# Performance work log

Hardware: AMD Instinct MI355X
Metric: run time of the kernel (lower is better)

## Reference

```python
import jax, jax.numpy as jnp
import numpy as np

LOCAL_RANGE = 7  # module default local_range
NUM_HEADS = 8


def setup_inputs() -> dict:
    key = jax.random.key(0)
    k1, k2, k3 = jax.random.split(key, 3)
    B, S, D = 2, 2048, 512
    hidden_states = jax.random.normal(k1, (B, S, D), dtype=jnp.float32)
    scale = 1.0 / (D ** 0.5)
    Wq = jax.random.normal(k2, (D, D), dtype=jnp.float32) * scale
    Wk = jax.random.normal(k3, (D, D), dtype=jnp.float32) * scale
    return {"hidden_states": hidden_states, "Wq": Wq, "Wk": Wk}


def reference(hidden_states, Wq, Wk):
    B, S, D = hidden_states.shape
    H = NUM_HEADS
    dh = D // H
    # inner attention: only attn_weights matter (context_layer is overwritten)
    q = (hidden_states @ Wq).reshape(B, S, H, dh).transpose(0, 2, 1, 3)  # [B,H,S,dh]
    k = (hidden_states @ Wk).reshape(B, S, H, dh).transpose(0, 2, 1, 3)  # [B,H,S,dh]
    scores = jnp.einsum('bhid,bhjd->bhij', q, k) / (dh ** 0.5)          # [B,H,S,S]
    attn_weights = jax.nn.softmax(scores, axis=-1)
    # band-diagonal local mask: |i-j| <= local_range (vectorized form of the python loop)
    idx = jnp.arange(S)
    band = (jnp.abs(idx[:, None] - idx[None, :]) <= LOCAL_RANGE).astype(attn_weights.dtype)  # [S,S]
    local_w = attn_weights * band
    local_w = local_w / (jnp.sum(local_w, axis=-1, keepdims=True) + 1e-6)
    # context = matmul(local_attn_weights, hidden_states): per-head contraction
    context = jnp.einsum('bhij,bjd->bhid', local_w, hidden_states)       # [B,H,S,D]
    return context
```

## Files before the change

### kernel.cpp

```cpp
#include <hip/hip_runtime.h>
#include <hip/hip_bf16.h>
#include <math.h>

#define SEQ   2048
#define DIM   512
#define NH    8
#define DH    64
#define LR    7

typedef __bf16 bf16_t;
typedef __bf16 bf16x8 __attribute__((ext_vector_type(8)));
typedef float  f32x4  __attribute__((ext_vector_type(4)));

__global__ __launch_bounds__(256) void wt_convert(
    const float* __restrict__ Wq, const float* __restrict__ Wk,
    bf16_t* __restrict__ Wt)
{
    __shared__ float tile[64][68];
    const int tid = threadIdx.x;
    const int k0 = blockIdx.x * 64;
    const int n0 = blockIdx.y * 64;
    const float* W = (n0 < DIM) ? Wq : Wk;
    const int nn0 = n0 & (DIM - 1);

    #pragma unroll
    for (int ph = 0; ph < 4; ++ph) {
        const int kk = ph * 16 + (tid >> 4);
        const int nn = (tid & 15) * 4;
        const float4 v = *(const float4*)(W + (size_t)(k0 + kk) * DIM + nn0 + nn);
        tile[kk][nn + 0] = v.x; tile[kk][nn + 1] = v.y;
        tile[kk][nn + 2] = v.z; tile[kk][nn + 3] = v.w;
    }
    __syncthreads();
    #pragma unroll
    for (int ph = 0; ph < 4; ++ph) {
        const int nn = ph * 16 + (tid >> 4);
        const int kk = (tid & 15) * 4;
        union { bf16_t b[4]; ushort4 u; } cv;
        #pragma unroll
        for (int u = 0; u < 4; ++u) cv.b[u] = (bf16_t)tile[kk + u][nn];
        *(ushort4*)(Wt + (size_t)(n0 + nn) * DIM + k0 + kk) = cv.u;
    }
}

__global__ __launch_bounds__(256) void qk_gemm_mfma(
    const float* __restrict__ A,
    const bf16_t* __restrict__ Bt,
    float* __restrict__ C)
{
    __shared__ bf16_t As[128][32];
    __shared__ bf16_t Bs[128][32];

    const int tid  = threadIdx.x;
    const int wave = tid >> 6;
    const int lane = tid & 63;
    const int l15  = lane & 15;
    const int quad = lane >> 4;
    const int wm   = (wave >> 1) * 64;
    const int wn   = (wave & 1) * 64;
    const int m0   = blockIdx.x * 128;
    const int n0   = blockIdx.y * 128;

    const int sm = tid >> 1;
    const int kh = (tid & 1) * 16;

    f32x4 acc[4][4] = {};

    for (int k0 = 0; k0 < DIM; k0 += 32) {
        {
            const float* ap = A + (size_t)(m0 + sm) * DIM + k0 + kh;
            const float4 f0 = *(const float4*)(ap + 0);
            const float4 f1 = *(const float4*)(ap + 4);
            const float4 f2 = *(const float4*)(ap + 8);
            const float4 f3 = *(const float4*)(ap + 12);
            union { bf16_t b[8]; uint4 u; } c0, c1;
            c0.b[0]=(bf16_t)f0.x; c0.b[1]=(bf16_t)f0.y; c0.b[2]=(bf16_t)f0.z; c0.b[3]=(bf16_t)f0.w;
            c0.b[4]=(bf16_t)f1.x; c0.b[5]=(bf16_t)f1.y; c0.b[6]=(bf16_t)f1.z; c0.b[7]=(bf16_t)f1.w;
            c1.b[0]=(bf16_t)f2.x; c1.b[1]=(bf16_t)f2.y; c1.b[2]=(bf16_t)f2.z; c1.b[3]=(bf16_t)f2.w;
            c1.b[4]=(bf16_t)f3.x; c1.b[5]=(bf16_t)f3.y; c1.b[6]=(bf16_t)f3.z; c1.b[7]=(bf16_t)f3.w;
            *(uint4*)&As[sm][kh + 0] = c0.u;
            *(uint4*)&As[sm][kh + 8] = c1.u;
        }
        {
            const uint4* bp = (const uint4*)(Bt + (size_t)(n0 + sm) * DIM + k0 + kh);
            *(uint4*)&Bs[sm][kh + 0] = bp[0];
            *(uint4*)&Bs[sm][kh + 8] = bp[1];
        }
        __syncthreads();

        bf16x8 af[4], bfv[4];
        #pragma unroll
        for (int t = 0; t < 4; ++t)
            af[t] = *(const bf16x8*)&As[wm + t * 16 + l15][quad * 8];
        #pragma unroll
        for (int t = 0; t < 4; ++t)
            bfv[t] = *(const bf16x8*)&Bs[wn + t * 16 + l15][quad * 8];

        #pragma unroll
        for (int mi = 0; mi < 4; ++mi)
            #pragma unroll
            for (int ni = 0; ni < 4; ++ni)
                acc[mi][ni] = __builtin_amdgcn_mfma_f32_16x16x32_bf16(
                    af[mi], bfv[ni], acc[mi][ni], 0, 0, 0);
        __syncthreads();
    }

    #pragma unroll
    for (int mi = 0; mi < 4; ++mi) {
        #pragma unroll
        for (int ni = 0; ni < 4; ++ni) {
            const int col = n0 + wn + ni * 16 + l15;
            #pragma unroll
            for (int r = 0; r < 4; ++r) {
                const int row = m0 + wm + mi * 16 + quad * 4 + r;
                C[(size_t)row * 1024 + col] = acc[mi][ni][r];
            }
        }
    }
}

#define TI 8
#define NROW (TI + 2 * LR)

__global__ __launch_bounds__(256) void local_attn2(
    const float* __restrict__ hs,
    const float* __restrict__ qk,
    float* __restrict__ out)
{
    __shared__ float hst[NROW][DIM + 4];
    __shared__ float sw[NH * TI][17];
    __shared__ float wn[NH * TI][17];

    const int tid = threadIdx.x;
    const int i0  = blockIdx.x * TI;
    const int b   = blockIdx.y;

    {
        const float4* hs4 = (const float4*)(hs + (size_t)b * SEQ * DIM);
        #pragma unroll
        for (int it = 0; it < (NROW * DIM / 4) / 256; ++it) {
            const int idx = it * 256 + tid;
            const int r   = idx >> 7;
            const int c4  = idx & 127;
            int jg = i0 - LR + r;
            jg = jg < 0 ? 0 : (jg > SEQ - 1 ? SEQ - 1 : jg);
            const float4 v = hs4[(size_t)jg * (DIM / 4) + c4];
            *(float4*)&hst[r][c4 * 4] = v;
        }
    }

    {
        const int pair = tid >> 2;
        const int h  = pair >> 3;
        const int ii = pair & (TI - 1);
        const int jq = tid & 3;
        const int i  = i0 + ii;
        const float4* qp = (const float4*)(qk + (size_t)(b * SEQ + i) * 1024 + h * DH);
        float4 q[DH / 4];
        #pragma unroll
        for (int u = 0; u < DH / 4; ++u) q[u] = qp[u];
        #pragma unroll
        for (int j = jq * 4; j < jq * 4 + 4 && j < 15; ++j) {
            const int jg = i - LR + j;
            float s = -1e30f;
            if (jg >= 0 && jg < SEQ) {
                const float4* kp = (const float4*)(qk + (size_t)(b * SEQ + jg) * 1024 + DIM + h * DH);
                float a = 0.f;
                #pragma unroll
                for (int u = 0; u < DH / 4; ++u) {
                    const float4 kv = kp[u];
                    a += q[u].x * kv.x + q[u].y * kv.y + q[u].z * kv.z + q[u].w * kv.w;
                }
                s = a * 0.125f;
            }
            sw[pair][j] = s;
        }
    }
    __syncthreads();

    if (tid < NH * TI) {
        float v[15], m = -1e30f;
        #pragma unroll
        for (int j = 0; j < 15; ++j) { v[j] = sw[tid][j]; m = fmaxf(m, v[j]); }
        float sum = 0.f;
        #pragma unroll
        for (int j = 0; j < 15; ++j) { v[j] = __expf(v[j] - m); sum += v[j]; }
        const float inv = 1.f / sum;
        #pragma unroll
        for (int j = 0; j < 15; ++j) wn[tid][j] = v[j] * inv;
    }
    __syncthreads();

    {
        const int h  = tid >> 5;
        const int iq = (tid >> 4) & 1;
        const int dg = tid & 15;

        float wreg[4][15];
        #pragma unroll
        for (int t = 0; t < 4; ++t) {
            const int pair = h * TI + iq * 4 + t;
            #pragma unroll
            for (int j = 0; j < 15; ++j) wreg[t][j] = wn[pair][j];
        }

        const int r0 = iq * 4;
        float* op = out + ((size_t)(b * NH + h) * SEQ + i0 + iq * 4) * DIM;

        for (int c = 0; c < DIM / 64; ++c) {
            const int dbase = c * 64 + dg * 4;
            float4 a0 = {0,0,0,0}, a1 = {0,0,0,0}, a2 = {0,0,0,0}, a3 = {0,0,0,0};
            #pragma unroll
            for (int rr = 0; rr < 18; ++rr) {
                const float4 v = *(const float4*)&hst[r0 + rr][dbase];
                if (rr <= 14) {
                    const float w = wreg[0][rr];
                    a0.x += w * v.x; a0.y += w * v.y; a0.z += w * v.z; a0.w += w * v.w;
                }
                if (rr >= 1 && rr <= 15) {
                    const float w = wreg[1][rr - 1];
                    a1.x += w * v.x; a1.y += w * v.y; a1.z += w * v.z; a1.w += w * v.w;
                }
                if (rr >= 2 && rr <= 16) {
                    const float w = wreg[2][rr - 2];
                    a2.x += w * v.x; a2.y += w * v.y; a2.z += w * v.z; a2.w += w * v.w;
                }
                if (rr >= 3) {
                    const float w = wreg[3][rr - 3];
                    a3.x += w * v.x; a3.y += w * v.y; a3.z += w * v.z; a3.w += w * v.w;
                }
            }
            *(float4*)(op + (size_t)0 * DIM + dbase) = a0;
            *(float4*)(op + (size_t)1 * DIM + dbase) = a1;
            *(float4*)(op + (size_t)2 * DIM + dbase) = a2;
            *(float4*)(op + (size_t)3 * DIM + dbase) = a3;
        }
    }
}

extern "C" void kernel_launch(void* const* d_in, const int* in_sizes, int n_in,
                              void* d_out, int out_size, void* d_ws, size_t ws_size,
                              hipStream_t stream)
{
    const float* hs = (const float*)d_in[0];
    const float* Wq = (const float*)d_in[1];
    const float* Wk = (const float*)d_in[2];
    float* out = (float*)d_out;

    const int B = in_sizes[0] / (SEQ * DIM);
    const int M = B * SEQ;

    bf16_t* Wt = (bf16_t*)d_ws;
    float*  qk = (float*)((char*)d_ws + (1 << 20));

    wt_convert<<<dim3(DIM / 64, 2 * DIM / 64), 256, 0, stream>>>(Wq, Wk, Wt);
    qk_gemm_mfma<<<dim3(M / 128, 1024 / 128), 256, 0, stream>>>(hs, Wt, qk);
    local_attn2<<<dim3(SEQ / TI, B), 256, 0, stream>>>(hs, qk, out);
}
```

Before: 127.9 us.

## Pre-convert activations to bf16, use direct global-to-LDS loads, stage Q/K band in LDS

Merges weight transposition with a new pass that converts hidden_states to bf16, so the QK GEMM reads bf16 activations through global_load_lds direct-to-LDS copies instead of converting fp32 in the loop. The GEMM M-tile is halved to 64 rows, which doubles the number of blocks. The local attention kernel stages the K band and the Q rows in shared memory so the score loop reads LDS instead of global memory, then reuses the same buffer for the hidden-state band. The cost is an extra 4 MB bf16 write and read, plus more LDS use per attention block.

```diff
diff --git a/kernel.cpp b/kernel.cpp
--- a/kernel.cpp
+++ b/kernel.cpp
@@ -12,14 +12,33 @@
 typedef __bf16 bf16x8 __attribute__((ext_vector_type(8)));
 typedef float  f32x4  __attribute__((ext_vector_type(4)));
 
-__global__ __launch_bounds__(256) void wt_convert(
+typedef __attribute__((address_space(3))) void  lds_void;
+typedef __attribute__((address_space(1))) const void gbl_cvoid;
+
+__global__ __launch_bounds__(256) void prep(
+    const float* __restrict__ hs,
     const float* __restrict__ Wq, const float* __restrict__ Wk,
+    bf16_t* __restrict__ hsb,
     bf16_t* __restrict__ Wt)
 {
+    const int tid = threadIdx.x;
+    const int bx  = blockIdx.x;
+
+    if (bx < 1024) {
+        const size_t base = ((size_t)bx * 256 + tid) * 8;
+        const float4 f0 = *(const float4*)(hs + base);
+        const float4 f1 = *(const float4*)(hs + base + 4);
+        union { bf16_t b[8]; uint4 u; } cv;
+        cv.b[0]=(bf16_t)f0.x; cv.b[1]=(bf16_t)f0.y; cv.b[2]=(bf16_t)f0.z; cv.b[3]=(bf16_t)f0.w;
+        cv.b[4]=(bf16_t)f1.x; cv.b[5]=(bf16_t)f1.y; cv.b[6]=(bf16_t)f1.z; cv.b[7]=(bf16_t)f1.w;
+        *(uint4*)(hsb + base) = cv.u;
+        return;
+    }
+
     __shared__ float tile[64][68];
-    const int tid = threadIdx.x;
-    const int k0 = blockIdx.x * 64;
-    const int n0 = blockIdx.y * 64;
+    const int t  = bx - 1024;
+    const int k0 = (t & 7) * 64;
+    const int n0 = (t >> 3) * 64;
     const float* W = (n0 < DIM) ? Wq : Wk;
     const int nn0 = n0 & (DIM - 1);
 
@@ -44,11 +63,11 @@
 }
 
 __global__ __launch_bounds__(256) void qk_gemm_mfma(
-    const float* __restrict__ A,
+    const bf16_t* __restrict__ A,
     const bf16_t* __restrict__ Bt,
     float* __restrict__ C)
 {
-    __shared__ bf16_t As[128][32];
+    __shared__ bf16_t As[64][32];
     __shared__ bf16_t Bs[128][32];
 
     const int tid  = threadIdx.x;
@@ -56,48 +75,40 @@
     const int lane = tid & 63;
     const int l15  = lane & 15;
     const int quad = lane >> 4;
-    const int wm   = (wave >> 1) * 64;
+    const int wm   = (wave >> 1) * 32;
     const int wn   = (wave & 1) * 64;
-    const int m0   = blockIdx.x * 128;
+    const int m0   = blockIdx.x * 64;
     const int n0   = blockIdx.y * 128;
 
-    const int sm = tid >> 1;
-    const int kh = (tid & 1) * 16;
-
-    f32x4 acc[4][4] = {};
+    const int srow = lane >> 2;
+    const int scol = (lane & 3) * 8;
+
+    const bf16_t* agp = A  + (size_t)(m0 + wave * 16 + srow) * DIM + scol;
+    const bf16_t* bgp = Bt + (size_t)(n0 + wave * 32 + srow) * DIM + scol;
+    bf16_t* alp = &As[wave * 16][0];
+    bf16_t* blp = &Bs[wave * 32][0];
+
+    f32x4 acc[2][4] = {};
 
     for (int k0 = 0; k0 < DIM; k0 += 32) {
-        {
-            const float* ap = A + (size_t)(m0 + sm) * DIM + k0 + kh;
-            const float4 f0 = *(const float4*)(ap + 0);
-            const float4 f1 = *(const float4*)(ap + 4);
-            const float4 f2 = *(const float4*)(ap + 8);
-            const float4 f3 = *(const float4*)(ap + 12);
-            union { bf16_t b[8]; uint4 u; } c0, c1;
-            c0.b[0]=(bf16_t)f0.x; c0.b[1]=(bf16_t)f0.y; c0.b[2]=(bf16_t)f0.z; c0.b[3]=(bf16_t)f0.w;
-            c0.b[4]=(bf16_t)f1.x; c0.b[5]=(bf16_t)f1.y; c0.b[6]=(bf16_t)f1.z; c0.b[7]=(bf16_t)f1.w;
-            c1.b[0]=(bf16_t)f2.x; c1.b[1]=(bf16_t)f2.y; c1.b[2]=(bf16_t)f2.z; c1.b[3]=(bf16_t)f2.w;
-            c1.b[4]=(bf16_t)f3.x; c1.b[5]=(bf16_t)f3.y; c1.b[6]=(bf16_t)f3.z; c1.b[7]=(bf16_t)f3.w;
-            *(uint4*)&As[sm][kh + 0] = c0.u;
-            *(uint4*)&As[sm][kh + 8] = c1.u;
-        }
-        {
-            const uint4* bp = (const uint4*)(Bt + (size_t)(n0 + sm) * DIM + k0 + kh);
-            *(uint4*)&Bs[sm][kh + 0] = bp[0];
-            *(uint4*)&Bs[sm][kh + 8] = bp[1];
-        }
+        __builtin_amdgcn_global_load_lds((gbl_cvoid*)(agp + k0),
+                                         (lds_void*)alp, 16, 0, 0);
+        __builtin_amdgcn_global_load_lds((gbl_cvoid*)(bgp + k0),
+                                         (lds_void*)blp, 16, 0, 0);
+        __builtin_amdgcn_global_load_lds((gbl_cvoid*)(bgp + 16 * DIM + k0),
+                                         (lds_void*)(blp + 16 * 32), 16, 0, 0);
         __syncthreads();
 
-        bf16x8 af[4], bfv[4];
-        #pragma unroll
-        for (int t = 0; t < 4; ++t)
+        bf16x8 af[2], bfv[4];
+        #pragma unroll
+        for (int t = 0; t < 2; ++t)
             af[t] = *(const bf16x8*)&As[wm + t * 16 + l15][quad * 8];
         #pragma unroll
         for (int t = 0; t < 4; ++t)
             bfv[t] = *(const bf16x8*)&Bs[wn + t * 16 + l15][quad * 8];
 
         #pragma unroll
-        for (int mi = 0; mi < 4; ++mi)
+        for (int mi = 0; mi < 2; ++mi)
             #pragma unroll
             for (int ni = 0; ni < 4; ++ni)
                 acc[mi][ni] = __builtin_amdgcn_mfma_f32_16x16x32_bf16(
@@ -106,7 +117,7 @@
     }
 
     #pragma unroll
-    for (int mi = 0; mi < 4; ++mi) {
+    for (int mi = 0; mi < 2; ++mi) {
         #pragma unroll
         for (int ni = 0; ni < 4; ++ni) {
             const int col = n0 + wn + ni * 16 + l15;
@@ -122,32 +133,39 @@
 #define TI 8
 #define NROW (TI + 2 * LR)
 
-__global__ __launch_bounds__(256) void local_attn2(
+__global__ __launch_bounds__(256) void local_attn3(
     const float* __restrict__ hs,
     const float* __restrict__ qk,
     float* __restrict__ out)
 {
-    __shared__ float hst[NROW][DIM + 4];
-    __shared__ float sw[NH * TI][17];
-    __shared__ float wn[NH * TI][17];
+    __shared__ float band[NROW][DIM + 4];
+    __shared__ float qst[TI][DIM + 4];
+    __shared__ float sw[NH * TI][16];
+    __shared__ float wn[NH * TI][16];
 
     const int tid = threadIdx.x;
     const int i0  = blockIdx.x * TI;
     const int b   = blockIdx.y;
 
     {
-        const float4* hs4 = (const float4*)(hs + (size_t)b * SEQ * DIM);
-        #pragma unroll
-        for (int it = 0; it < (NROW * DIM / 4) / 256; ++it) {
-            const int idx = it * 256 + tid;
-            const int r   = idx >> 7;
-            const int c4  = idx & 127;
+        for (int idx = tid; idx < NROW * 128; idx += 256) {
+            const int r  = idx >> 7;
+            const int c4 = idx & 127;
             int jg = i0 - LR + r;
             jg = jg < 0 ? 0 : (jg > SEQ - 1 ? SEQ - 1 : jg);
-            const float4 v = hs4[(size_t)jg * (DIM / 4) + c4];
-            *(float4*)&hst[r][c4 * 4] = v;
-        }
-    }
+            const float4 v = *(const float4*)(qk + (size_t)(b * SEQ + jg) * 1024 + DIM + c4 * 4);
+            *(float4*)&band[r][c4 * 4] = v;
+        }
+        {
+            const int r  = tid >> 5;
+            const int c4 = (tid & 31) * 4;
+            const float4* src = (const float4*)(qk + (size_t)(b * SEQ + i0 + r) * 1024) + c4;
+            #pragma unroll
+            for (int u = 0; u < 4; ++u)
+                *(float4*)&qst[r][(c4 + u) * 4] = src[u];
+        }
+    }
+    __syncthreads();
 
     {
         const int pair = tid >> 2;
@@ -155,21 +173,21 @@
         const int ii = pair & (TI - 1);
         const int jq = tid & 3;
         const int i  = i0 + ii;
-        const float4* qp = (const float4*)(qk + (size_t)(b * SEQ + i) * 1024 + h * DH);
-        float4 q[DH / 4];
-        #pragma unroll
-        for (int u = 0; u < DH / 4; ++u) q[u] = qp[u];
-        #pragma unroll
-        for (int j = jq * 4; j < jq * 4 + 4 && j < 15; ++j) {
+        const float4* qp = (const float4*)&qst[ii][h * DH];
+        #pragma unroll
+        for (int jj = 0; jj < 4; ++jj) {
+            const int j = jq * 4 + jj;
+            if (j >= 15) break;
             const int jg = i - LR + j;
             float s = -1e30f;
             if (jg >= 0 && jg < SEQ) {
-                const float4* kp = (const float4*)(qk + (size_t)(b * SEQ + jg) * 1024 + DIM + h * DH);
+                const float4* kp = (const float4*)&band[ii + j][h * DH];
                 float a = 0.f;
                 #pragma unroll
                 for (int u = 0; u < DH / 4; ++u) {
+                    const float4 qv = qp[u];
                     const float4 kv = kp[u];
-                    a += q[u].x * kv.x + q[u].y * kv.y + q[u].z * kv.z + q[u].w * kv.w;
+                    a += qv.x * kv.x + qv.y * kv.y + qv.z * kv.z + qv.w * kv.w;
                 }
                 s = a * 0.125f;
             }
@@ -189,6 +207,16 @@
         #pragma unroll
         for (int j = 0; j < 15; ++j) wn[tid][j] = v[j] * inv;
     }
+    {
+        for (int idx = tid; idx < NROW * 128; idx += 256) {
+            const int r  = idx >> 7;
+            const int c4 = idx & 127;
+            int jg = i0 - LR + r;
+            jg = jg < 0 ? 0 : (jg > SEQ - 1 ? SEQ - 1 : jg);
+            const float4 v = *(const float4*)(hs + ((size_t)b * SEQ + jg) * DIM + c4 * 4);
+            *(float4*)&band[r][c4 * 4] = v;
+        }
+    }
     __syncthreads();
 
     {
@@ -212,7 +240,7 @@
             float4 a0 = {0,0,0,0}, a1 = {0,0,0,0}, a2 = {0,0,0,0}, a3 = {0,0,0,0};
             #pragma unroll
             for (int rr = 0; rr < 18; ++rr) {
-                const float4 v = *(const float4*)&hst[r0 + rr][dbase];
+                const float4 v = *(const float4*)&band[r0 + rr][dbase];
                 if (rr <= 14) {
                     const float w = wreg[0][rr];
                     a0.x += w * v.x; a0.y += w * v.y; a0.z += w * v.z; a0.w += w * v.w;
@@ -250,10 +278,11 @@
     const int B = in_sizes[0] / (SEQ * DIM);
     const int M = B * SEQ;
 
-    bf16_t* Wt = (bf16_t*)d_ws;
-    float*  qk = (float*)((char*)d_ws + (1 << 20));
-
-    wt_convert<<<dim3(DIM / 64, 2 * DIM / 64), 256, 0, stream>>>(Wq, Wk, Wt);
-    qk_gemm_mfma<<<dim3(M / 128, 1024 / 128), 256, 0, stream>>>(hs, Wt, qk);
-    local_attn2<<<dim3(SEQ / TI, B), 256, 0, stream>>>(hs, qk, out);
-}
+    bf16_t* hsb = (bf16_t*)d_ws;
+    bf16_t* Wt  = (bf16_t*)((char*)d_ws + (4 << 20));
+    float*  qk  = (float*)((char*)d_ws + (5 << 20));
+
+    prep<<<1024 + 128, 256, 0, stream>>>(hs, Wq, Wk, hsb, Wt);
+    qk_gemm_mfma<<<dim3(M / 64, 1024 / 128), 256, 0, stream>>>(hsb, Wt, qk);
+    local_attn3<<<dim3(SEQ / TI, B), 256, 0, stream>>>(hs, qk, out);
+}
```

Result: faster. 117.1 us (-8.4%).
